# Performance work log

Measured on AMD Instinct MI355X. Metric: run time of the kernel, lower is better.

The kernel has to match this reference:

```python
import jax, jax.numpy as jnp
import numpy as np

B, T, C, H = 4, 4096, 1024, 128

def setup_inputs() -> dict:
    key = jax.random.key(0)
    kx, kq, kk, kv = jax.random.split(key, 4)
    s = 1.0 / np.sqrt(C)  # linear-layer-like init scale
    return {
        "x": jax.random.normal(kx, (B, T, C), dtype=jnp.float32),
        "Wq": jax.random.normal(kq, (C, H), dtype=jnp.float32) * s,
        "Wk": jax.random.normal(kk, (C, H), dtype=jnp.float32) * s,
        "Wv": jax.random.normal(kv, (C, H), dtype=jnp.float32) * s,
    }

def reference(x, Wq, Wk, Wv):
    # q,k,v: [B,T,H]
    q = jnp.einsum('btc,ch->bth', x, Wq)
    k = jnp.einsum('btc,ch->bth', x, Wk)
    v = jnp.einsum('btc,ch->bth', x, Wv)
    # scores: [B,T,T]  (NOTE: source applies no 1/sqrt(H) scaling)
    wei = jnp.einsum('bth,bih->bti', q, k)
    t = x.shape[1]
    causal = jnp.tril(jnp.ones((t, t), dtype=bool))
    wei = jnp.where(causal, wei, -jnp.inf)
    probs = jax.nn.softmax(wei, axis=-1)
    out = jnp.einsum('btj,bjh->bth', probs, v)
    return out
```

## Files before the change

### kernel.cpp

```cpp
#include <hip/hip_runtime.h>

#define B_ 4
#define T_ 4096
#define C_ 1024
#define H_ 128

typedef __attribute__((ext_vector_type(8))) __bf16 bf16x8;
typedef __attribute__((ext_vector_type(8))) unsigned short u16x8;
typedef __attribute__((ext_vector_type(4))) float f32x4;

__device__ __forceinline__ unsigned short f2bf(float f) {
  unsigned int u = __float_as_uint(f);
  return (unsigned short)((u + 0x7FFFu + ((u >> 16) & 1u)) >> 16);
}
__device__ __forceinline__ float bf2f(unsigned short h) {
  return __uint_as_float((unsigned)h << 16);
}
__device__ __forceinline__ bf16x8 ldb8(const unsigned short* p) {
  return *(const bf16x8*)(const void*)p;
}
__device__ __forceinline__ void async16(void* lds, const void* g) {
  __builtin_amdgcn_global_load_lds(
      (const __attribute__((address_space(1))) unsigned int*)g,
      (__attribute__((address_space(3))) unsigned int*)lds, 16, 0, 0);
}
__device__ __forceinline__ void split8a(const float* f, bf16x8& hi, bf16x8& lo) {
  u16x8 h, l;
#pragma unroll
  for (int j = 0; j < 8; j++) {
    h[j] = f2bf(f[j]);
    l[j] = f2bf(f[j] - bf2f(h[j]));
  }
  hi = __builtin_bit_cast(bf16x8, h);
  lo = __builtin_bit_cast(bf16x8, l);
}


__global__ void wt_k(const float* __restrict__ Wq, const float* __restrict__ Wk,
                     const float* __restrict__ Wv, unsigned short* __restrict__ Whi,
                     unsigned short* __restrict__ Wlo) {
  __shared__ float tile[32][33];
  int m = blockIdx.z;
  const float* W = (m == 0) ? Wq : ((m == 1) ? Wk : Wv);
  int c0 = blockIdx.x * 32, h0 = blockIdx.y * 32;
  int tx = threadIdx.x, ty = threadIdx.y;
#pragma unroll
  for (int i = 0; i < 4; i++)
    tile[ty + 8 * i][tx] = W[(size_t)(c0 + ty + 8 * i) * H_ + h0 + tx];
  __syncthreads();
  size_t base = (size_t)m * H_ * C_;
#pragma unroll
  for (int i = 0; i < 4; i++) {
    float f = tile[tx][ty + 8 * i];
    unsigned short hi = f2bf(f);
    int h = h0 + ty + 8 * i;
    int kg = c0 + tx;
    int w0 = kg >> 6, c = (kg >> 3) & 7, e = kg & 7;
    size_t idx = base + (size_t)h * C_ + w0 * 64 + ((c + (h & 7)) & 7) * 8 + e;
    Whi[idx] = hi;
    if (m < 2) Wlo[idx] = f2bf(f - bf2f(hi));
  }
}

__global__ __launch_bounds__(256, 3) void qkv_k(
    const float* __restrict__ x, const unsigned short* __restrict__ Whi,
    const unsigned short* __restrict__ Wlo, unsigned short* __restrict__ Qhi,
    unsigned short* __restrict__ Qlo, unsigned short* __restrict__ Khf,
    unsigned short* __restrict__ Klf, unsigned short* __restrict__ Vf) {
  int m = blockIdx.x % 3;
  int r0 = (blockIdx.x / 3) * 64;
  __shared__ __align__(16) float sx[64 * 64];
  __shared__ __align__(16) unsigned short swh[128 * 64];
  __shared__ __align__(16) unsigned short swl[128 * 64];
  int tid = threadIdx.x;
  int lane = tid & 63, wave = tid >> 6;
  int l15 = lane & 15, quad = lane >> 4;
  const unsigned short* Wmh = Whi + (size_t)m * H_ * C_;
  const unsigned short* Wml = Wlo + (size_t)m * H_ * C_;
  f32x4 acc[8];
#pragma unroll
  for (int n = 0; n < 8; n++) acc[n] = (f32x4){0.f, 0.f, 0.f, 0.f};

  for (int k0 = 0; k0 < C_; k0 += 64) {
    __syncthreads();
#pragma unroll
    for (int i = 0; i < 4; i++) {
      int s = (wave * 4 + i) * 64 + lane;
      {
        int tr = s >> 4, p = s & 15;
        async16((unsigned short*)sx + (size_t)(wave * 4 + i) * 512,
                x + (size_t)(r0 + tr) * C_ + k0 + ((p - tr) & 15) * 4);
      }
      {
        int hr = s >> 3, p = s & 7;
        async16(swh + (size_t)(wave * 4 + i) * 512,
                Wmh + (size_t)hr * C_ + k0 + p * 8);
        if (m < 2)
          async16(swl + (size_t)(wave * 4 + i) * 512,
                  Wml + (size_t)hr * C_ + k0 + p * 8);
      }
    }
    __syncthreads();
#pragma unroll
    for (int kk = 0; kk < 2; kk++) {
      float xa[8];
#pragma unroll
      for (int half = 0; half < 2; half++) {
        int p = (kk * 8 + quad * 2 + half + l15) & 15;
        *(f32x4*)&xa[half * 4] =
            *(const f32x4*)(const void*)(sx + (wave * 16 + l15) * 64 + p * 4);
      }
      bf16x8 ahi, alo;
      split8a(xa, ahi, alo);
      if (m < 2) {
#pragma unroll
        for (int n = 0; n < 8; n++) {
          int p = (kk * 4 + quad + l15) & 7;
          bf16x8 bhi = ldb8(swh + (n * 16 + l15) * 64 + p * 8);
          bf16x8 blo = ldb8(swl + (n * 16 + l15) * 64 + p * 8);
          acc[n] = __builtin_amdgcn_mfma_f32_16x16x32_bf16(ahi, bhi, acc[n], 0, 0, 0);
          acc[n] = __builtin_amdgcn_mfma_f32_16x16x32_bf16(alo, bhi, acc[n], 0, 0, 0);
          acc[n] = __builtin_amdgcn_mfma_f32_16x16x32_bf16(ahi, blo, acc[n], 0, 0, 0);
        }
      } else {
#pragma unroll
        for (int n = 0; n < 8; n++) {
          int p = (kk * 4 + quad + l15) & 7;
          bf16x8 bhi = ldb8(swh + (n * 16 + l15) * 64 + p * 8);
          acc[n] = __builtin_amdgcn_mfma_f32_16x16x32_bf16(ahi, bhi, acc[n], 0, 0, 0);
        }
      }
    }
  }
  int ob = r0 + wave * 16 + quad * 4;
  if (m == 0) {
#pragma unroll
    for (int n8 = 0; n8 < 8; n8++)
#pragma unroll
      for (int r = 0; r < 4; r++) {
        float f = acc[n8][r];
        unsigned short hi = f2bf(f);
        size_t idx = (size_t)(ob + r) * H_ + n8 * 16 + l15;
        Qhi[idx] = hi;
        Qlo[idx] = f2bf(f - bf2f(hi));
      }
  } else if (m == 1) {
#pragma unroll
    for (int n8 = 0; n8 < 8; n8++)
#pragma unroll
      for (int r = 0; r < 4; r++) {
        int gr = ob + r;
        int bb = gr >> 12, t = gr & (T_ - 1);
        int kt = t >> 6, tr = t & 63, nf = tr >> 4, lk = tr & 15;
        int h = n8 * 16 + l15;
        int kkf = h >> 5, qk = (h >> 3) & 3, e = h & 7;
        size_t idx = (size_t)bb * T_ * H_ +
                     (size_t)((kt * 16 + nf * 4 + kkf) * 64 + qk * 16 + lk) * 8 + e;
        float f = acc[n8][r];
        unsigned short hi = f2bf(f);
        Khf[idx] = hi;
        Klf[idx] = f2bf(f - bf2f(hi));
      }
  } else {
#pragma unroll
    for (int n8 = 0; n8 < 8; n8++)
#pragma unroll
      for (int r = 0; r < 4; r++) {
        int gr = ob + r;
        int bb = gr >> 12, t = gr & (T_ - 1);
        int kt = t >> 6, ks = (t >> 5) & 1, qv = (t >> 3) & 3, jj = t & 7;
        size_t idx = (size_t)bb * T_ * H_ +
                     (size_t)((kt * 16 + ks * 8 + n8) * 64 + qv * 16 + l15) * 8 + jj;
        Vf[idx] = f2bf(acc[n8][r]);
      }
  }
}

#define PP2 40
__global__ __launch_bounds__(256, 2) void flash2_k(
    const unsigned short* __restrict__ Qhi, const unsigned short* __restrict__ Qlo,
    const unsigned short* __restrict__ Khf, const unsigned short* __restrict__ Klf,
    const unsigned short* __restrict__ Vf, float* __restrict__ opart,
    float2* __restrict__ mlpart) {
  __shared__ __align__(16) unsigned short skh[2][4096];
  __shared__ __align__(16) unsigned short skl[2][4096];
  __shared__ __align__(16) unsigned short sv[2][4096];
  __shared__ __align__(16) unsigned short pb[4][16 * PP2];
  int tid = threadIdx.x;
  int wave = tid >> 6, lane = tid & 63;
  int l15 = lane & 15, quad = lane >> 4;

  int g = blockIdx.x & 7;
  int j = blockIdx.x >> 3;
  int b = g >> 1, sp = g & 1;
  int p = 63 - j;
  int q0 = p << 6;
  int ktB = sp ? (p + 1) : 0;
  int nt = p + 1;
  size_t boff = (size_t)b * T_ * H_;
  const unsigned short* Khb = Khf + boff;
  const unsigned short* Klb = Klf + boff;
  const unsigned short* Vb = Vf + boff;

  bf16x8 qh[4], ql[4];
  {
    const unsigned short* qrh =
        Qhi + boff + (size_t)(q0 + wave * 16 + l15) * H_ + quad * 8;
    const unsigned short* qrl =
        Qlo + boff + (size_t)(q0 + wave * 16 + l15) * H_ + quad * 8;
#pragma unroll
    for (int kk = 0; kk < 4; kk++) {
      qh[kk] = ldb8(qrh + kk * 32);
      ql[kk] = ldb8(qrl + kk * 32);
    }
  }
  f32x4 o[8];
#pragma unroll
  for (int n = 0; n < 8; n++) o[n] = (f32x4){0.f, 0.f, 0.f, 0.f};
  float mr[4] = {-1e30f, -1e30f, -1e30f, -1e30f};
  float lr[4] = {0.f, 0.f, 0.f, 0.f};

  int rmin = q0 + wave * 16;
  unsigned short* pbw = pb[wave];
  int ch = wave * 2;

#define STAGE(kt32_, d_)                                                        \
  {                                                                             \
    size_t gbase = (size_t)(kt32_)*4096 + (size_t)ch * 512 + (size_t)lane * 8;  \
    async16(&skh[d_][ch * 512], Khb + gbase);                                   \
    async16(&skh[d_][(ch + 1) * 512], Khb + gbase + 512);                       \
    async16(&skl[d_][ch * 512], Klb + gbase);                                   \
    async16(&skl[d_][(ch + 1) * 512], Klb + gbase + 512);                       \
    async16(&sv[d_][ch * 512], Vb + gbase);                                     \
    async16(&sv[d_][(ch + 1) * 512], Vb + gbase + 512);                         \
  }

  STAGE(ktB, 0);
  int cur = 0;
  for (int it = 0; it < nt; ++it) {
    int kt32 = ktB + it;
    if (it + 1 < nt) {
      STAGE(kt32 + 1, cur ^ 1);
      asm volatile("s_waitcnt vmcnt(6)" ::: "memory");
    } else {
      asm volatile("s_waitcnt vmcnt(0)" ::: "memory");
    }
    __builtin_amdgcn_s_barrier();
    int c0 = kt32 << 5;
    if (c0 <= rmin + 15) {
      f32x4 s[2];
#pragma unroll
      for (int n16 = 0; n16 < 2; ++n16) s[n16] = (f32x4){0.f, 0.f, 0.f, 0.f};
#pragma unroll
      for (int n16 = 0; n16 < 2; ++n16) {
        bf16x8 kh[4], kl[4];
#pragma unroll
        for (int kk = 0; kk < 4; kk++) {
          kh[kk] = ldb8(&skh[cur][(n16 * 4 + kk) * 512 + lane * 8]);
          kl[kk] = ldb8(&skl[cur][(n16 * 4 + kk) * 512 + lane * 8]);
        }
#pragma unroll
        for (int kk = 0; kk < 4; kk++) {
          s[n16] = __builtin_amdgcn_mfma_f32_16x16x32_bf16(qh[kk], kh[kk], s[n16], 0, 0, 0);
          s[n16] = __builtin_amdgcn_mfma_f32_16x16x32_bf16(ql[kk], kh[kk], s[n16], 0, 0, 0);
          s[n16] = __builtin_amdgcn_mfma_f32_16x16x32_bf16(qh[kk], kl[kk], s[n16], 0, 0, 0);
        }
      }
      if (c0 + 31 > rmin) {
#pragma unroll
        for (int n16 = 0; n16 < 2; ++n16) {
          int col = c0 + n16 * 16 + l15;
#pragma unroll
          for (int r = 0; r < 4; r++)
            if (col > rmin + quad * 4 + r) s[n16][r] = -1e30f;
        }
      }
      float mnew[4];
#pragma unroll
      for (int r = 0; r < 4; r++) mnew[r] = fmaxf(s[0][r], s[1][r]);
#pragma unroll
      for (int off = 1; off < 16; off <<= 1)
#pragma unroll
        for (int r = 0; r < 4; r++) mnew[r] = fmaxf(mnew[r], __shfl_xor(mnew[r], off));
      float alpha[4];
#pragma unroll
      for (int r = 0; r < 4; r++) {
        float mi = fmaxf(mr[r], mnew[r]);
        alpha[r] = __expf(mr[r] - mi);
        mr[r] = mi;
      }
      float rs[4];
#pragma unroll
      for (int n16 = 0; n16 < 2; ++n16)
#pragma unroll
        for (int r = 0; r < 4; r++) s[n16][r] = __expf(s[n16][r] - mr[r]);
#pragma unroll
      for (int r = 0; r < 4; r++) rs[r] = s[0][r] + s[1][r];
#pragma unroll
      for (int off = 1; off < 16; off <<= 1)
#pragma unroll
        for (int r = 0; r < 4; r++) rs[r] += __shfl_xor(rs[r], off);
#pragma unroll
      for (int r = 0; r < 4; r++) lr[r] = lr[r] * alpha[r] + rs[r];
#pragma unroll
      for (int n = 0; n < 8; n++)
#pragma unroll
        for (int r = 0; r < 4; r++) o[n][r] *= alpha[r];
      asm volatile("s_waitcnt lgkmcnt(0)" ::: "memory");
#pragma unroll
      for (int n16 = 0; n16 < 2; ++n16)
#pragma unroll
        for (int r = 0; r < 4; r++)
          pbw[(quad * 4 + r) * PP2 + n16 * 16 + l15] = f2bf(s[n16][r]);
      asm volatile("s_waitcnt lgkmcnt(0)" ::: "memory");
      bf16x8 pa = ldb8(pbw + l15 * PP2 + quad * 8);
#pragma unroll
      for (int nv = 0; nv < 8; ++nv) {
        bf16x8 vf = ldb8(&sv[cur][nv * 512 + lane * 8]);
        o[nv] = __builtin_amdgcn_mfma_f32_16x16x32_bf16(pa, vf, o[nv], 0, 0, 0);
      }
    }
    __builtin_amdgcn_s_barrier();
    cur ^= 1;
  }
#undef STAGE

  size_t obase = (size_t)((b * 64 + p) * 2 + sp) * (64 * 128);
  int wr = wave * 16 + quad * 4;
#pragma unroll
  for (int n = 0; n < 8; n++)
#pragma unroll
    for (int r = 0; r < 4; r++)
      opart[obase + (size_t)(wr + r) * 128 + n * 16 + l15] = o[n][r];
  if (l15 == 0) {
    size_t mbase = (size_t)((b * 64 + p) * 2 + sp) * 64;
#pragma unroll
    for (int r = 0; r < 4; r++)
      mlpart[mbase + wr + r] = make_float2(mr[r], lr[r]);
  }
}

__global__ __launch_bounds__(256) void comb_k(const float* __restrict__ opart,
                                              const float2* __restrict__ mlpart,
                                              float* __restrict__ out) {
  int gid = blockIdx.x * 256 + threadIdx.x;
  int row = gid >> 4;
  int c0 = (gid & 15) << 3;
  int b = row >> 12, t = row & (T_ - 1);
  int p = t >> 6, r = t & 63;
  size_t mi = (size_t)(b * 64 + p) * 2 * 64 + r;
  float2 ml0 = mlpart[mi], ml1 = mlpart[mi + 64];
  float M = fmaxf(ml0.x, ml1.x);
  float w0 = __expf(ml0.x - M), w1 = __expf(ml1.x - M);
  float invL = 1.0f / (w0 * ml0.y + w1 * ml1.y);
  size_t o0 = ((size_t)(b * 64 + p) * 2 * 64 + r) * 128 + c0;
  size_t o1 = o0 + 64 * 128;
  f32x4 a0 = *(const f32x4*)(const void*)(opart + o0) * w0 +
             *(const f32x4*)(const void*)(opart + o1) * w1;
  f32x4 a1 = *(const f32x4*)(const void*)(opart + o0 + 4) * w0 +
             *(const f32x4*)(const void*)(opart + o1 + 4) * w1;
  float* op = out + ((size_t)b * T_ + t) * H_ + c0;
  *(f32x4*)(void*)op = a0 * invL;
  *(f32x4*)(void*)(op + 4) = a1 * invL;
}

extern "C" void kernel_launch(void* const* d_in, const int* in_sizes, int n_in,
                              void* d_out, int out_size, void* d_ws, size_t ws_size,
                              hipStream_t stream) {
  const float* x  = (const float*)d_in[0];
  const float* Wq = (const float*)d_in[1];
  const float* Wk = (const float*)d_in[2];
  const float* Wv = (const float*)d_in[3];
  const size_t BTH = (size_t)B_ * T_ * H_;
  unsigned short* Whi = (unsigned short*)d_ws;
  unsigned short* Wlo = Whi + 3 * H_ * C_;
  unsigned short* Vf  = Wlo + 2 * H_ * C_;
  unsigned short* Qhi = Vf + BTH;
  unsigned short* Qlo = Qhi + BTH;
  unsigned short* Khf = Qlo + BTH;
  unsigned short* Klf = Khf + BTH;
  float* opart = (float*)(void*)(Klf + BTH);
  float2* mlpart = (float2*)(void*)(opart + (size_t)B_ * 64 * 2 * 64 * 128);
  float* out = (float*)d_out;

  wt_k<<<dim3(32, 4, 3), dim3(32, 8), 0, stream>>>(Wq, Wk, Wv, Whi, Wlo);
  qkv_k<<<3 * (B_ * T_ / 64), 256, 0, stream>>>(x, Whi, Wlo, Qhi, Qlo, Khf, Klf, Vf);
  flash2_k<<<512, 256, 0, stream>>>(Qhi, Qlo, Khf, Klf, Vf, opart, mlpart);
  comb_k<<<(B_ * T_ * 16) / 256, 256, 0, stream>>>(opart, mlpart, out);
}
```

Baseline: 252.7 us.

## Process 128-row query tiles with two 16-row slices per wave, split KV four ways

The flash attention kernel now gives each wave two 16-row query slices (128 rows per block) that share each staged K/V tile. This halves the K/V LDS traffic and global staging per query row. The KV range is split into four partitions per query tile instead of two, so the grid stays at 512 blocks. The combine kernel now merges four partials per row. The cost is higher register pressure from doubled Q fragments and accumulators, which may spill at the two-blocks-per-CU launch bound. It also adds more partial-output traffic and extra work in the combine step.

New measurement: 239.5 us. 1.06x faster.

```diff
diff --git a/kernel.cpp b/kernel.cpp
--- a/kernel.cpp
+++ b/kernel.cpp
@@ -176,8 +176,43 @@
   }
 }
 
+__device__ __forceinline__ void online_sm(f32x4* s, float* mr, float* lr,
+                                          f32x4* o) {
+  float mnew[4];
+#pragma unroll
+  for (int r = 0; r < 4; r++) mnew[r] = fmaxf(s[0][r], s[1][r]);
+#pragma unroll
+  for (int off = 1; off < 16; off <<= 1)
+#pragma unroll
+    for (int r = 0; r < 4; r++) mnew[r] = fmaxf(mnew[r], __shfl_xor(mnew[r], off));
+  float alpha[4];
+#pragma unroll
+  for (int r = 0; r < 4; r++) {
+    float mi = fmaxf(mr[r], mnew[r]);
+    alpha[r] = __expf(mr[r] - mi);
+    mr[r] = mi;
+  }
+#pragma unroll
+  for (int n16 = 0; n16 < 2; ++n16)
+#pragma unroll
+    for (int r = 0; r < 4; r++) s[n16][r] = __expf(s[n16][r] - mr[r]);
+  float rs[4];
+#pragma unroll
+  for (int r = 0; r < 4; r++) rs[r] = s[0][r] + s[1][r];
+#pragma unroll
+  for (int off = 1; off < 16; off <<= 1)
+#pragma unroll
+    for (int r = 0; r < 4; r++) rs[r] += __shfl_xor(rs[r], off);
+#pragma unroll
+  for (int r = 0; r < 4; r++) lr[r] = lr[r] * alpha[r] + rs[r];
+#pragma unroll
+  for (int n = 0; n < 8; n++)
+#pragma unroll
+    for (int r = 0; r < 4; r++) o[n][r] *= alpha[r];
+}
+
 #define PP2 40
-__global__ __launch_bounds__(256, 2) void flash2_k(
+__global__ __launch_bounds__(256, 2) void flash3_k(
     const unsigned short* __restrict__ Qhi, const unsigned short* __restrict__ Qlo,
     const unsigned short* __restrict__ Khf, const unsigned short* __restrict__ Klf,
     const unsigned short* __restrict__ Vf, float* __restrict__ opart,
@@ -185,43 +220,51 @@
   __shared__ __align__(16) unsigned short skh[2][4096];
   __shared__ __align__(16) unsigned short skl[2][4096];
   __shared__ __align__(16) unsigned short sv[2][4096];
-  __shared__ __align__(16) unsigned short pb[4][16 * PP2];
+  __shared__ __align__(16) unsigned short pb[4][2][16 * PP2];
   int tid = threadIdx.x;
   int wave = tid >> 6, lane = tid & 63;
   int l15 = lane & 15, quad = lane >> 4;
 
-  int g = blockIdx.x & 7;
-  int j = blockIdx.x >> 3;
-  int b = g >> 1, sp = g & 1;
-  int p = 63 - j;
-  int q0 = p << 6;
-  int ktB = sp ? (p + 1) : 0;
+  int n = blockIdx.x;
+  int p = 31 - (n >> 4);
+  int g = n & 15;
+  int sp = g >> 2, b = g & 3;
+  int q0 = p << 7;
+  int ktB = sp * (p + 1);
   int nt = p + 1;
   size_t boff = (size_t)b * T_ * H_;
   const unsigned short* Khb = Khf + boff;
   const unsigned short* Klb = Klf + boff;
   const unsigned short* Vb = Vf + boff;
 
-  bf16x8 qh[4], ql[4];
+  bf16x8 qh0[4], ql0[4], qh1[4], ql1[4];
   {
     const unsigned short* qrh =
-        Qhi + boff + (size_t)(q0 + wave * 16 + l15) * H_ + quad * 8;
+        Qhi + boff + (size_t)(q0 + wave * 32 + l15) * H_ + quad * 8;
     const unsigned short* qrl =
-        Qlo + boff + (size_t)(q0 + wave * 16 + l15) * H_ + quad * 8;
+        Qlo + boff + (size_t)(q0 + wave * 32 + l15) * H_ + quad * 8;
 #pragma unroll
     for (int kk = 0; kk < 4; kk++) {
-      qh[kk] = ldb8(qrh + kk * 32);
-      ql[kk] = ldb8(qrl + kk * 32);
-    }
-  }
-  f32x4 o[8];
-#pragma unroll
-  for (int n = 0; n < 8; n++) o[n] = (f32x4){0.f, 0.f, 0.f, 0.f};
-  float mr[4] = {-1e30f, -1e30f, -1e30f, -1e30f};
-  float lr[4] = {0.f, 0.f, 0.f, 0.f};
-
-  int rmin = q0 + wave * 16;
-  unsigned short* pbw = pb[wave];
+      qh0[kk] = ldb8(qrh + kk * 32);
+      ql0[kk] = ldb8(qrl + kk * 32);
+      qh1[kk] = ldb8(qrh + 16 * H_ + kk * 32);
+      ql1[kk] = ldb8(qrl + 16 * H_ + kk * 32);
+    }
+  }
+  f32x4 o0[8], o1[8];
+#pragma unroll
+  for (int nn = 0; nn < 8; nn++) {
+    o0[nn] = (f32x4){0.f, 0.f, 0.f, 0.f};
+    o1[nn] = (f32x4){0.f, 0.f, 0.f, 0.f};
+  }
+  float mr0[4] = {-1e30f, -1e30f, -1e30f, -1e30f};
+  float mr1[4] = {-1e30f, -1e30f, -1e30f, -1e30f};
+  float lr0[4] = {0.f, 0.f, 0.f, 0.f};
+  float lr1[4] = {0.f, 0.f, 0.f, 0.f};
+
+  int rmin = q0 + wave * 32;
+  unsigned short* pb0 = pb[wave][0];
+  unsigned short* pb1 = pb[wave][1];
   int ch = wave * 2;
 
 #define STAGE(kt32_, d_)                                                        \
@@ -246,11 +289,16 @@
       asm volatile("s_waitcnt vmcnt(0)" ::: "memory");
     }
     __builtin_amdgcn_s_barrier();
-    int c0 = kt32 << 5;
-    if (c0 <= rmin + 15) {
-      f32x4 s[2];
-#pragma unroll
-      for (int n16 = 0; n16 < 2; ++n16) s[n16] = (f32x4){0.f, 0.f, 0.f, 0.f};
+    int c0k = kt32 << 5;
+    bool t1a = (c0k <= rmin + 31);
+    bool t0a = (c0k <= rmin + 15);
+    if (t1a) {
+      f32x4 s0[2], s1[2];
+#pragma unroll
+      for (int n16 = 0; n16 < 2; ++n16) {
+        s0[n16] = (f32x4){0.f, 0.f, 0.f, 0.f};
+        s1[n16] = (f32x4){0.f, 0.f, 0.f, 0.f};
+      }
 #pragma unroll
       for (int n16 = 0; n16 < 2; ++n16) {
         bf16x8 kh[4], kl[4];
@@ -261,63 +309,57 @@
         }
 #pragma unroll
         for (int kk = 0; kk < 4; kk++) {
-          s[n16] = __builtin_amdgcn_mfma_f32_16x16x32_bf16(qh[kk], kh[kk], s[n16], 0, 0, 0);
-          s[n16] = __builtin_amdgcn_mfma_f32_16x16x32_bf16(ql[kk], kh[kk], s[n16], 0, 0, 0);
-          s[n16] = __builtin_amdgcn_mfma_f32_16x16x32_bf16(qh[kk], kl[kk], s[n16], 0, 0, 0);
-        }
-      }
-      if (c0 + 31 > rmin) {
+          s0[n16] = __builtin_amdgcn_mfma_f32_16x16x32_bf16(qh0[kk], kh[kk], s0[n16], 0, 0, 0);
+          s0[n16] = __builtin_amdgcn_mfma_f32_16x16x32_bf16(ql0[kk], kh[kk], s0[n16], 0, 0, 0);
+          s0[n16] = __builtin_amdgcn_mfma_f32_16x16x32_bf16(qh0[kk], kl[kk], s0[n16], 0, 0, 0);
+          s1[n16] = __builtin_amdgcn_mfma_f32_16x16x32_bf16(qh1[kk], kh[kk], s1[n16], 0, 0, 0);
+          s1[n16] = __builtin_amdgcn_mfma_f32_16x16x32_bf16(ql1[kk], kh[kk], s1[n16], 0, 0, 0);
+          s1[n16] = __builtin_amdgcn_mfma_f32_16x16x32_bf16(qh1[kk], kl[kk], s1[n16], 0, 0, 0);
+        }
+      }
+      if (c0k + 31 > rmin + 16) {
 #pragma unroll
         for (int n16 = 0; n16 < 2; ++n16) {
-          int col = c0 + n16 * 16 + l15;
+          int col = c0k + n16 * 16 + l15;
 #pragma unroll
           for (int r = 0; r < 4; r++)
-            if (col > rmin + quad * 4 + r) s[n16][r] = -1e30f;
-        }
-      }
-      float mnew[4];
-#pragma unroll
-      for (int r = 0; r < 4; r++) mnew[r] = fmaxf(s[0][r], s[1][r]);
-#pragma unroll
-      for (int off = 1; off < 16; off <<= 1)
-#pragma unroll
-        for (int r = 0; r < 4; r++) mnew[r] = fmaxf(mnew[r], __shfl_xor(mnew[r], off));
-      float alpha[4];
-#pragma unroll
-      for (int r = 0; r < 4; r++) {
-        float mi = fmaxf(mr[r], mnew[r]);
-        alpha[r] = __expf(mr[r] - mi);
-        mr[r] = mi;
-      }
-      float rs[4];
+            if (col > rmin + 16 + quad * 4 + r) s1[n16][r] = -1e30f;
+        }
+      }
+      if (t0a && c0k + 31 > rmin) {
+#pragma unroll
+        for (int n16 = 0; n16 < 2; ++n16) {
+          int col = c0k + n16 * 16 + l15;
+#pragma unroll
+          for (int r = 0; r < 4; r++)
+            if (col > rmin + quad * 4 + r) s0[n16][r] = -1e30f;
+        }
+      }
+      online_sm(s1, mr1, lr1, o1);
+      if (t0a) online_sm(s0, mr0, lr0, o0);
+      asm volatile("s_waitcnt lgkmcnt(0)" ::: "memory");
 #pragma unroll
       for (int n16 = 0; n16 < 2; ++n16)
 #pragma unroll
-        for (int r = 0; r < 4; r++) s[n16][r] = __expf(s[n16][r] - mr[r]);
-#pragma unroll
-      for (int r = 0; r < 4; r++) rs[r] = s[0][r] + s[1][r];
-#pragma unroll
-      for (int off = 1; off < 16; off <<= 1)
-#pragma unroll
-        for (int r = 0; r < 4; r++) rs[r] += __shfl_xor(rs[r], off);
-#pragma unroll
-      for (int r = 0; r < 4; r++) lr[r] = lr[r] * alpha[r] + rs[r];
-#pragma unroll
-      for (int n = 0; n < 8; n++)
-#pragma unroll
-        for (int r = 0; r < 4; r++) o[n][r] *= alpha[r];
+        for (int r = 0; r < 4; r++)
+          pb1[(quad * 4 + r) * PP2 + n16 * 16 + l15] = f2bf(s1[n16][r]);
+      if (t0a) {
+#pragma unroll
+        for (int n16 = 0; n16 < 2; ++n16)
+#pragma unroll
+          for (int r = 0; r < 4; r++)
+            pb0[(quad * 4 + r) * PP2 + n16 * 16 + l15] = f2bf(s0[n16][r]);
+      }
       asm volatile("s_waitcnt lgkmcnt(0)" ::: "memory");
-#pragma unroll
-      for (int n16 = 0; n16 < 2; ++n16)
-#pragma unroll
-        for (int r = 0; r < 4; r++)
-          pbw[(quad * 4 + r) * PP2 + n16 * 16 + l15] = f2bf(s[n16][r]);
-      asm volatile("s_waitcnt lgkmcnt(0)" ::: "memory");
-      bf16x8 pa = ldb8(pbw + l15 * PP2 + quad * 8);
+      bf16x8 pa1 = ldb8(pb1 + l15 * PP2 + quad * 8);
+      bf16x8 pa0;
+      if (t0a) pa0 = ldb8(pb0 + l15 * PP2 + quad * 8);
 #pragma unroll
       for (int nv = 0; nv < 8; ++nv) {
         bf16x8 vf = ldb8(&sv[cur][nv * 512 + lane * 8]);
-        o[nv] = __builtin_amdgcn_mfma_f32_16x16x32_bf16(pa, vf, o[nv], 0, 0, 0);
+        o1[nv] = __builtin_amdgcn_mfma_f32_16x16x32_bf16(pa1, vf, o1[nv], 0, 0, 0);
+        if (t0a)
+          o0[nv] = __builtin_amdgcn_mfma_f32_16x16x32_bf16(pa0, vf, o0[nv], 0, 0, 0);
       }
     }
     __builtin_amdgcn_s_barrier();
@@ -325,18 +367,22 @@
   }
 #undef STAGE
 
-  size_t obase = (size_t)((b * 64 + p) * 2 + sp) * (64 * 128);
-  int wr = wave * 16 + quad * 4;
-#pragma unroll
-  for (int n = 0; n < 8; n++)
-#pragma unroll
-    for (int r = 0; r < 4; r++)
-      opart[obase + (size_t)(wr + r) * 128 + n * 16 + l15] = o[n][r];
+  size_t obase = (size_t)((b * 32 + p) * 4 + sp) * (128 * 128);
+  size_t mbase = (size_t)((b * 32 + p) * 4 + sp) * 128;
+  int wr0 = wave * 32 + quad * 4;
+#pragma unroll
+  for (int nn = 0; nn < 8; nn++)
+#pragma unroll
+    for (int r = 0; r < 4; r++) {
+      opart[obase + (size_t)(wr0 + r) * 128 + nn * 16 + l15] = o0[nn][r];
+      opart[obase + (size_t)(wr0 + 16 + r) * 128 + nn * 16 + l15] = o1[nn][r];
+    }
   if (l15 == 0) {
-    size_t mbase = (size_t)((b * 64 + p) * 2 + sp) * 64;
-#pragma unroll
-    for (int r = 0; r < 4; r++)
-      mlpart[mbase + wr + r] = make_float2(mr[r], lr[r]);
+#pragma unroll
+    for (int r = 0; r < 4; r++) {
+      mlpart[mbase + wr0 + r] = make_float2(mr0[r], lr0[r]);
+      mlpart[mbase + wr0 + 16 + r] = make_float2(mr1[r], lr1[r]);
+    }
   }
 }
 
@@ -347,18 +393,26 @@
   int row = gid >> 4;
   int c0 = (gid & 15) << 3;
   int b = row >> 12, t = row & (T_ - 1);
-  int p = t >> 6, r = t & 63;
-  size_t mi = (size_t)(b * 64 + p) * 2 * 64 + r;
-  float2 ml0 = mlpart[mi], ml1 = mlpart[mi + 64];
-  float M = fmaxf(ml0.x, ml1.x);
-  float w0 = __expf(ml0.x - M), w1 = __expf(ml1.x - M);
-  float invL = 1.0f / (w0 * ml0.y + w1 * ml1.y);
-  size_t o0 = ((size_t)(b * 64 + p) * 2 * 64 + r) * 128 + c0;
-  size_t o1 = o0 + 64 * 128;
-  f32x4 a0 = *(const f32x4*)(const void*)(opart + o0) * w0 +
-             *(const f32x4*)(const void*)(opart + o1) * w1;
-  f32x4 a1 = *(const f32x4*)(const void*)(opart + o0 + 4) * w0 +
-             *(const f32x4*)(const void*)(opart + o1 + 4) * w1;
+  int p = t >> 7, r = t & 127;
+  size_t base = (size_t)(b * 32 + p) * 4;
+  float2 ml[4];
+#pragma unroll
+  for (int s = 0; s < 4; s++) ml[s] = mlpart[base * 128 + s * 128 + r];
+  float M = fmaxf(fmaxf(ml[0].x, ml[1].x), fmaxf(ml[2].x, ml[3].x));
+  float w[4], L = 0.f;
+#pragma unroll
+  for (int s = 0; s < 4; s++) {
+    w[s] = __expf(ml[s].x - M);
+    L += w[s] * ml[s].y;
+  }
+  float invL = 1.0f / L;
+  f32x4 a0 = (f32x4){0.f, 0.f, 0.f, 0.f}, a1 = a0;
+#pragma unroll
+  for (int s = 0; s < 4; s++) {
+    const float* src = opart + (base + s) * (128 * 128) + (size_t)r * 128 + c0;
+    a0 += *(const f32x4*)(const void*)src * w[s];
+    a1 += *(const f32x4*)(const void*)(src + 4) * w[s];
+  }
   float* op = out + ((size_t)b * T_ + t) * H_ + c0;
   *(f32x4*)(void*)op = a0 * invL;
   *(f32x4*)(void*)(op + 4) = a1 * invL;
@@ -380,11 +434,11 @@
   unsigned short* Khf = Qlo + BTH;
   unsigned short* Klf = Khf + BTH;
   float* opart = (float*)(void*)(Klf + BTH);
-  float2* mlpart = (float2*)(void*)(opart + (size_t)B_ * 64 * 2 * 64 * 128);
+  float2* mlpart = (float2*)(void*)(opart + 4 * BTH);
   float* out = (float*)d_out;
 
   wt_k<<<dim3(32, 4, 3), dim3(32, 8), 0, stream>>>(Wq, Wk, Wv, Whi, Wlo);
   qkv_k<<<3 * (B_ * T_ / 64), 256, 0, stream>>>(x, Whi, Wlo, Qhi, Qlo, Khf, Klf, Vf);
-  flash2_k<<<512, 256, 0, stream>>>(Qhi, Qlo, Khf, Klf, Vf, opart, mlpart);
+  flash3_k<<<512, 256, 0, stream>>>(Qhi, Qlo, Khf, Klf, Vf, opart, mlpart);
   comb_k<<<(B_ * T_ * 16) / 256, 256, 0, stream>>>(opart, mlpart, out);
 }
```
